# Performance work log

Measured on AMD Instinct MI355X. Metric: run time of the kernel, lower is better.

The kernel has to match this reference:

```python
import jax, jax.numpy as jnp
import numpy as np

B = 262144          # batch
D = 128             # in_dim == out_dim
BS = 16             # block size
K = 8               # number of blocks
RANK = 4            # low-rank blocks' rank
DENSE = np.array([0, 3, 6])   # block ids with mode 'dense'
DIAG = np.array([1, 4, 7])    # block ids with mode 'diagonal'
LR = np.array([2, 5])         # block ids with mode 'lowrank'
EPS = 1e-8


def setup_inputs() -> dict:
    key = jax.random.key(0)
    k1, k2, k3, k4, k5 = jax.random.split(key, 5)
    x = jax.random.normal(k1, (B, D), dtype=jnp.float32)
    # dense blocks: torch init is identity (d_in==d_out); add noise so math is non-trivial
    W_dense = jnp.eye(BS, dtype=jnp.float32)[None] + 0.1 * jax.random.normal(k2, (len(DENSE), BS, BS), dtype=jnp.float32)
    # diagonal blocks: torch init is ones; perturb slightly
    s_diag = 1.0 + 0.1 * jax.random.normal(k3, (len(DIAG), BS), dtype=jnp.float32)
    # lowrank blocks: xavier-uniform-like scale
    lim = float(np.sqrt(6.0 / (BS + RANK)))
    U = jax.random.uniform(k4, (len(LR), BS, RANK), dtype=jnp.float32, minval=-lim, maxval=lim)
    V = jax.random.uniform(k5, (len(LR), BS, RANK), dtype=jnp.float32, minval=-lim, maxval=lim)
    return {"x": x, "W_dense": W_dense, "s_diag": s_diag, "U": U, "V": V}


def reference(x, W_dense, s_diag, U, V):
    # blocks are contiguous [16*j, 16*(j+1)), so gather == reshape to [B, K, BS]
    x3 = x.reshape(B, K, BS)
    # dense blocks: torch Linear y = x @ W.T, W is [d_out, d_in]
    yd = jnp.einsum('bkd,kod->bko', x3[:, DENSE], W_dense)
    # diagonal blocks: elementwise scale
    yg = x3[:, DIAG] * s_diag
    # lowrank blocks: x @ V @ U.T
    yl = jnp.einsum('bkr,kor->bko', jnp.einsum('bkd,kdr->bkr', x3[:, LR], V), U)
    y = jnp.zeros_like(x3).at[:, DENSE].set(yd).at[:, DIAG].set(yg).at[:, LR].set(yl)
    y = y.reshape(B, D)
    # l2 normalize (normalize=True)
    norm = jnp.linalg.norm(y, axis=-1, keepdims=True)
    return y / (norm + EPS)
```

## Files before the change

### kernel.cpp

```cpp
#include <hip/hip_runtime.h>

#define BATCH   262144
#define DDIM    128
#define GRID    2048
#define NITER   8
#define FLUSH   4

template <int CTRL>
__device__ __forceinline__ float fdpp(float v) {
    int i = __builtin_bit_cast(int, v);
    i = __builtin_amdgcn_mov_dpp(i, CTRL, 0xF, 0xF, true);
    return __builtin_bit_cast(float, i);
}
__device__ __forceinline__ float fswz16(float v) {
    int i = __builtin_bit_cast(int, v);
    i = __builtin_amdgcn_ds_swizzle(i, 0x401F);
    return __builtin_bit_cast(float, i);
}

__global__ __launch_bounds__(256, 4) void bdla_kernel(
    const float* __restrict__ x,
    const float* __restrict__ Wd,
    const float* __restrict__ sd,
    const float* __restrict__ U,
    const float* __restrict__ V,
    float* __restrict__ out)
{
    __shared__ float wl[1072];
    __shared__ float obuf[4][FLUSH][4][DDIM];

    const int tid = threadIdx.x;
    for (int i = tid; i < 768; i += 256) wl[i] = Wd[i];
    if (tid < 48)  wl[768 + tid] = sd[tid];
    if (tid < 128) wl[816 + tid] = U[tid];
    if (tid < 128) wl[944 + tid] = V[tid];
    __syncthreads();

    const int lane   = tid & 63;
    const int lane32 = lane & 31;
    const int half   = lane >> 5;
    const int w      = tid >> 6;
    const int j      = lane32 >> 2;
    const int sub    = lane32 & 3;
    const int mode   = j % 3;
    const int k      = j / 3;

    float A[4][16];
    if (mode == 0) {
        const float* wm = &wl[k * 256];
#pragma unroll
        for (int oo = 0; oo < 4; ++oo) {
            const int o = sub * 4 + oo;
#pragma unroll
            for (int m = 0; m < 4; ++m)
#pragma unroll
                for (int c = 0; c < 4; ++c)
                    A[oo][m * 4 + c] = wm[o * 16 + ((sub ^ m) * 4 + c)];
        }
    } else if (mode == 1) {
        const float* s = &wl[768 + k * 16];
#pragma unroll
        for (int oo = 0; oo < 4; ++oo)
#pragma unroll
            for (int m = 0; m < 4; ++m)
#pragma unroll
                for (int c = 0; c < 4; ++c)
                    A[oo][m * 4 + c] = (m == 0 && c == oo) ? s[sub * 4 + oo] : 0.0f;
    } else {
        const float* u = &wl[816 + k * 64];
        const float* v = &wl[944 + k * 64];
#pragma unroll
        for (int oo = 0; oo < 4; ++oo) {
            const int o = sub * 4 + oo;
#pragma unroll
            for (int m = 0; m < 4; ++m)
#pragma unroll
                for (int c = 0; c < 4; ++c) {
                    const int d = (sub ^ m) * 4 + c;
                    float acc = 0.0f;
#pragma unroll
                    for (int r = 0; r < 4; ++r)
                        acc += u[o * 4 + r] * v[d * 4 + r];
                    A[oo][m * 4 + c] = acc;
                }
        }
    }

#pragma unroll
    for (int oo = 0; oo < 4; ++oo)
#pragma unroll
        for (int t = 0; t < 16; ++t)
            asm volatile("" : "+v"(A[oo][t]));

    const int gw = blockIdx.x * 4 + w;
    const float* xbase = x + (size_t)(gw * 4 + half) * DDIM + lane32 * 4;
    const size_t istep = (size_t)(GRID * 4 * 4) * DDIM;

    float4 a0 = *(const float4*)(xbase);
    float4 b0 = *(const float4*)(xbase + 2 * DDIM);
    float4 a1 = *(const float4*)(xbase + istep);
    float4 b1 = *(const float4*)(xbase + istep + 2 * DDIM);

#pragma unroll
    for (int it = 0; it < NITER; ++it) {
        float4 a2, b2;
        if (it + 2 < NITER) {
            a2 = *(const float4*)(xbase + (size_t)(it + 2) * istep);
            b2 = *(const float4*)(xbase + (size_t)(it + 2) * istep + 2 * DDIM);
        }

        float ga[16], gb[16];
        ga[0] = a0.x; ga[1] = a0.y; ga[2] = a0.z; ga[3] = a0.w;
        gb[0] = b0.x; gb[1] = b0.y; gb[2] = b0.z; gb[3] = b0.w;
        ga[4]  = fdpp<0xB1>(a0.x); ga[5]  = fdpp<0xB1>(a0.y);
        ga[6]  = fdpp<0xB1>(a0.z); ga[7]  = fdpp<0xB1>(a0.w);
        gb[4]  = fdpp<0xB1>(b0.x); gb[5]  = fdpp<0xB1>(b0.y);
        gb[6]  = fdpp<0xB1>(b0.z); gb[7]  = fdpp<0xB1>(b0.w);
        ga[8]  = fdpp<0x4E>(a0.x); ga[9]  = fdpp<0x4E>(a0.y);
        ga[10] = fdpp<0x4E>(a0.z); ga[11] = fdpp<0x4E>(a0.w);
        gb[8]  = fdpp<0x4E>(b0.x); gb[9]  = fdpp<0x4E>(b0.y);
        gb[10] = fdpp<0x4E>(b0.z); gb[11] = fdpp<0x4E>(b0.w);
        ga[12] = fdpp<0x1B>(a0.x); ga[13] = fdpp<0x1B>(a0.y);
        ga[14] = fdpp<0x1B>(a0.z); ga[15] = fdpp<0x1B>(a0.w);
        gb[12] = fdpp<0x1B>(b0.x); gb[13] = fdpp<0x1B>(b0.y);
        gb[14] = fdpp<0x1B>(b0.z); gb[15] = fdpp<0x1B>(b0.w);

        float ya0 = 0.f, ya1 = 0.f, ya2 = 0.f, ya3 = 0.f;
        float yb0 = 0.f, yb1 = 0.f, yb2 = 0.f, yb3 = 0.f;
#pragma unroll
        for (int t = 0; t < 16; ++t) {
            ya0 = fmaf(A[0][t], ga[t], ya0);
            ya1 = fmaf(A[1][t], ga[t], ya1);
            ya2 = fmaf(A[2][t], ga[t], ya2);
            ya3 = fmaf(A[3][t], ga[t], ya3);
            yb0 = fmaf(A[0][t], gb[t], yb0);
            yb1 = fmaf(A[1][t], gb[t], yb1);
            yb2 = fmaf(A[2][t], gb[t], yb2);
            yb3 = fmaf(A[3][t], gb[t], yb3);
        }

        float ssa = ya0 * ya0 + ya1 * ya1 + ya2 * ya2 + ya3 * ya3;
        float ssb = yb0 * yb0 + yb1 * yb1 + yb2 * yb2 + yb3 * yb3;
        ssa += fdpp<0xB1>(ssa);  ssb += fdpp<0xB1>(ssb);
        ssa += fdpp<0x4E>(ssa);  ssb += fdpp<0x4E>(ssb);
        ssa += fdpp<0x141>(ssa); ssb += fdpp<0x141>(ssb);
        ssa += fdpp<0x140>(ssa); ssb += fdpp<0x140>(ssb);
        ssa += fswz16(ssa);      ssb += fswz16(ssb);
        const float inva = 1.0f / (sqrtf(ssa) + 1e-8f);
        const float invb = 1.0f / (sqrtf(ssb) + 1e-8f);

        float4 yva, yvb;
        yva.x = ya0 * inva; yva.y = ya1 * inva; yva.z = ya2 * inva; yva.w = ya3 * inva;
        yvb.x = yb0 * invb; yvb.y = yb1 * invb; yvb.z = yb2 * invb; yvb.w = yb3 * invb;

        float* wb = &obuf[w][it & (FLUSH - 1)][0][0];
        *(float4*)(wb + half * DDIM + lane32 * 4)       = yva;
        *(float4*)(wb + (half + 2) * DDIM + lane32 * 4) = yvb;

        if ((it & (FLUSH - 1)) == (FLUSH - 1)) {
            const int f = it >> 2;
#pragma unroll
            for (int s = 0; s < FLUSH; ++s) {
#pragma unroll
                for (int p = 0; p < 2; ++p) {
                    const float4 v =
                        *(const float4*)(&obuf[w][s][p * 2][0] + lane * 4);
                    const size_t row = (size_t)(f * FLUSH + s) * (GRID * 16)
                                     + gw * 4 + p * 2;
                    *(float4*)(out + row * DDIM + lane * 4) = v;
                }
            }
        }

        a0 = a1; b0 = b1; a1 = a2; b1 = b2;
    }
}

extern "C" void kernel_launch(void* const* d_in, const int* in_sizes, int n_in,
                              void* d_out, int out_size, void* d_ws, size_t ws_size,
                              hipStream_t stream) {
    const float* x  = (const float*)d_in[0];
    const float* Wd = (const float*)d_in[1];
    const float* sd = (const float*)d_in[2];
    const float* U  = (const float*)d_in[3];
    const float* V  = (const float*)d_in[4];
    float* out = (float*)d_out;
    (void)in_sizes; (void)n_in; (void)out_size; (void)d_ws; (void)ws_size;

    dim3 grid(GRID), block(256);
    hipLaunchKernelGGL(bdla_kernel, grid, block, 0, stream, x, Wd, sd, U, V, out);
}
```

Baseline: 280.7 us.

## Batch input loads into two phases of four and prefetch before weight setup

```diff
diff --git a/kernel.cpp b/kernel.cpp
--- a/kernel.cpp
+++ b/kernel.cpp
@@ -4,7 +4,7 @@
 #define DDIM    128
 #define GRID    2048
 #define NITER   8
-#define FLUSH   4
+#define PH      4
 
 template <int CTRL>
 __device__ __forceinline__ float fdpp(float v) {
@@ -18,7 +18,57 @@
     return __builtin_bit_cast(float, i);
 }
 
-__global__ __launch_bounds__(256, 4) void bdla_kernel(
+#define BDLA_BODY(A0, B0, WB)                                                 \
+    {                                                                         \
+        const float4 a0 = (A0);                                               \
+        const float4 b0 = (B0);                                               \
+        float ga[16], gb[16];                                                 \
+        ga[0] = a0.x; ga[1] = a0.y; ga[2] = a0.z; ga[3] = a0.w;               \
+        gb[0] = b0.x; gb[1] = b0.y; gb[2] = b0.z; gb[3] = b0.w;               \
+        ga[4]  = fdpp<0xB1>(a0.x); ga[5]  = fdpp<0xB1>(a0.y);                 \
+        ga[6]  = fdpp<0xB1>(a0.z); ga[7]  = fdpp<0xB1>(a0.w);                 \
+        gb[4]  = fdpp<0xB1>(b0.x); gb[5]  = fdpp<0xB1>(b0.y);                 \
+        gb[6]  = fdpp<0xB1>(b0.z); gb[7]  = fdpp<0xB1>(b0.w);                 \
+        ga[8]  = fdpp<0x4E>(a0.x); ga[9]  = fdpp<0x4E>(a0.y);                 \
+        ga[10] = fdpp<0x4E>(a0.z); ga[11] = fdpp<0x4E>(a0.w);                 \
+        gb[8]  = fdpp<0x4E>(b0.x); gb[9]  = fdpp<0x4E>(b0.y);                 \
+        gb[10] = fdpp<0x4E>(b0.z); gb[11] = fdpp<0x4E>(b0.w);                 \
+        ga[12] = fdpp<0x1B>(a0.x); ga[13] = fdpp<0x1B>(a0.y);                 \
+        ga[14] = fdpp<0x1B>(a0.z); ga[15] = fdpp<0x1B>(a0.w);                 \
+        gb[12] = fdpp<0x1B>(b0.x); gb[13] = fdpp<0x1B>(b0.y);                 \
+        gb[14] = fdpp<0x1B>(b0.z); gb[15] = fdpp<0x1B>(b0.w);                 \
+        float ya0 = 0.f, ya1 = 0.f, ya2 = 0.f, ya3 = 0.f;                     \
+        float yb0 = 0.f, yb1 = 0.f, yb2 = 0.f, yb3 = 0.f;                     \
+        _Pragma("unroll")                                                     \
+        for (int t = 0; t < 16; ++t) {                                        \
+            ya0 = fmaf(A[0][t], ga[t], ya0);                                  \
+            ya1 = fmaf(A[1][t], ga[t], ya1);                                  \
+            ya2 = fmaf(A[2][t], ga[t], ya2);                                  \
+            ya3 = fmaf(A[3][t], ga[t], ya3);                                  \
+            yb0 = fmaf(A[0][t], gb[t], yb0);                                  \
+            yb1 = fmaf(A[1][t], gb[t], yb1);                                  \
+            yb2 = fmaf(A[2][t], gb[t], yb2);                                  \
+            yb3 = fmaf(A[3][t], gb[t], yb3);                                  \
+        }                                                                     \
+        float ssa = ya0 * ya0 + ya1 * ya1 + ya2 * ya2 + ya3 * ya3;            \
+        float ssb = yb0 * yb0 + yb1 * yb1 + yb2 * yb2 + yb3 * yb3;            \
+        ssa += fdpp<0xB1>(ssa);  ssb += fdpp<0xB1>(ssb);                      \
+        ssa += fdpp<0x4E>(ssa);  ssb += fdpp<0x4E>(ssb);                      \
+        ssa += fdpp<0x141>(ssa); ssb += fdpp<0x141>(ssb);                     \
+        ssa += fdpp<0x140>(ssa); ssb += fdpp<0x140>(ssb);                     \
+        ssa += fswz16(ssa);      ssb += fswz16(ssb);                          \
+        const float inva = 1.0f / (sqrtf(ssa) + 1e-8f);                       \
+        const float invb = 1.0f / (sqrtf(ssb) + 1e-8f);                       \
+        float4 yva, yvb;                                                      \
+        yva.x = ya0 * inva; yva.y = ya1 * inva;                               \
+        yva.z = ya2 * inva; yva.w = ya3 * inva;                               \
+        yvb.x = yb0 * invb; yvb.y = yb1 * invb;                               \
+        yvb.z = yb2 * invb; yvb.w = yb3 * invb;                               \
+        *(float4*)((WB) + half * DDIM + lane32 * 4)       = yva;              \
+        *(float4*)((WB) + (half + 2) * DDIM + lane32 * 4) = yvb;              \
+    }
+
+__global__ __launch_bounds__(256, 3) void bdla_kernel(
     const float* __restrict__ x,
     const float* __restrict__ Wd,
     const float* __restrict__ sd,
@@ -27,7 +77,7 @@
     float* __restrict__ out)
 {
     __shared__ float wl[1072];
-    __shared__ float obuf[4][FLUSH][4][DDIM];
+    __shared__ float obuf[4][PH][4][DDIM];
 
     const int tid = threadIdx.x;
     for (int i = tid; i < 768; i += 256) wl[i] = Wd[i];
@@ -45,6 +95,17 @@
     const int mode   = j % 3;
     const int k      = j / 3;
 
+    const int gw = blockIdx.x * 4 + w;
+    const float* xbase = x + (size_t)(gw * 4 + half) * DDIM + lane32 * 4;
+    const size_t istep = (size_t)(GRID * 4 * 4) * DDIM;
+
+    float4 pa[PH], pb[PH];
+#pragma unroll
+    for (int s = 0; s < PH; ++s) {
+        pa[s] = *(const float4*)(xbase + (size_t)s * istep);
+        pb[s] = *(const float4*)(xbase + (size_t)s * istep + 2 * DDIM);
+    }
+
     float A[4][16];
     if (mode == 0) {
         const float* wm = &wl[k * 256];
@@ -85,94 +146,42 @@
                 }
         }
     }
-
 #pragma unroll
     for (int oo = 0; oo < 4; ++oo)
 #pragma unroll
         for (int t = 0; t < 16; ++t)
             asm volatile("" : "+v"(A[oo][t]));
 
-    const int gw = blockIdx.x * 4 + w;
-    const float* xbase = x + (size_t)(gw * 4 + half) * DDIM + lane32 * 4;
-    const size_t istep = (size_t)(GRID * 4 * 4) * DDIM;
-
-    float4 a0 = *(const float4*)(xbase);
-    float4 b0 = *(const float4*)(xbase + 2 * DDIM);
-    float4 a1 = *(const float4*)(xbase + istep);
-    float4 b1 = *(const float4*)(xbase + istep + 2 * DDIM);
-
-#pragma unroll
-    for (int it = 0; it < NITER; ++it) {
-        float4 a2, b2;
-        if (it + 2 < NITER) {
-            a2 = *(const float4*)(xbase + (size_t)(it + 2) * istep);
-            b2 = *(const float4*)(xbase + (size_t)(it + 2) * istep + 2 * DDIM);
-        }
-
-        float ga[16], gb[16];
-        ga[0] = a0.x; ga[1] = a0.y; ga[2] = a0.z; ga[3] = a0.w;
-        gb[0] = b0.x; gb[1] = b0.y; gb[2] = b0.z; gb[3] = b0.w;
-        ga[4]  = fdpp<0xB1>(a0.x); ga[5]  = fdpp<0xB1>(a0.y);
-        ga[6]  = fdpp<0xB1>(a0.z); ga[7]  = fdpp<0xB1>(a0.w);
-        gb[4]  = fdpp<0xB1>(b0.x); gb[5]  = fdpp<0xB1>(b0.y);
-        gb[6]  = fdpp<0xB1>(b0.z); gb[7]  = fdpp<0xB1>(b0.w);
-        ga[8]  = fdpp<0x4E>(a0.x); ga[9]  = fdpp<0x4E>(a0.y);
-        ga[10] = fdpp<0x4E>(a0.z); ga[11] = fdpp<0x4E>(a0.w);
-        gb[8]  = fdpp<0x4E>(b0.x); gb[9]  = fdpp<0x4E>(b0.y);
-        gb[10] = fdpp<0x4E>(b0.z); gb[11] = fdpp<0x4E>(b0.w);
-        ga[12] = fdpp<0x1B>(a0.x); ga[13] = fdpp<0x1B>(a0.y);
-        ga[14] = fdpp<0x1B>(a0.z); ga[15] = fdpp<0x1B>(a0.w);
-        gb[12] = fdpp<0x1B>(b0.x); gb[13] = fdpp<0x1B>(b0.y);
-        gb[14] = fdpp<0x1B>(b0.z); gb[15] = fdpp<0x1B>(b0.w);
-
-        float ya0 = 0.f, ya1 = 0.f, ya2 = 0.f, ya3 = 0.f;
-        float yb0 = 0.f, yb1 = 0.f, yb2 = 0.f, yb3 = 0.f;
-#pragma unroll
-        for (int t = 0; t < 16; ++t) {
-            ya0 = fmaf(A[0][t], ga[t], ya0);
-            ya1 = fmaf(A[1][t], ga[t], ya1);
-            ya2 = fmaf(A[2][t], ga[t], ya2);
-            ya3 = fmaf(A[3][t], ga[t], ya3);
-            yb0 = fmaf(A[0][t], gb[t], yb0);
-            yb1 = fmaf(A[1][t], gb[t], yb1);
-            yb2 = fmaf(A[2][t], gb[t], yb2);
-            yb3 = fmaf(A[3][t], gb[t], yb3);
-        }
-
-        float ssa = ya0 * ya0 + ya1 * ya1 + ya2 * ya2 + ya3 * ya3;
-        float ssb = yb0 * yb0 + yb1 * yb1 + yb2 * yb2 + yb3 * yb3;
-        ssa += fdpp<0xB1>(ssa);  ssb += fdpp<0xB1>(ssb);
-        ssa += fdpp<0x4E>(ssa);  ssb += fdpp<0x4E>(ssb);
-        ssa += fdpp<0x141>(ssa); ssb += fdpp<0x141>(ssb);
-        ssa += fdpp<0x140>(ssa); ssb += fdpp<0x140>(ssb);
-        ssa += fswz16(ssa);      ssb += fswz16(ssb);
-        const float inva = 1.0f / (sqrtf(ssa) + 1e-8f);
-        const float invb = 1.0f / (sqrtf(ssb) + 1e-8f);
-
-        float4 yva, yvb;
-        yva.x = ya0 * inva; yva.y = ya1 * inva; yva.z = ya2 * inva; yva.w = ya3 * inva;
-        yvb.x = yb0 * invb; yvb.y = yb1 * invb; yvb.z = yb2 * invb; yvb.w = yb3 * invb;
-
-        float* wb = &obuf[w][it & (FLUSH - 1)][0][0];
-        *(float4*)(wb + half * DDIM + lane32 * 4)       = yva;
-        *(float4*)(wb + (half + 2) * DDIM + lane32 * 4) = yvb;
-
-        if ((it & (FLUSH - 1)) == (FLUSH - 1)) {
-            const int f = it >> 2;
-#pragma unroll
-            for (int s = 0; s < FLUSH; ++s) {
-#pragma unroll
-                for (int p = 0; p < 2; ++p) {
-                    const float4 v =
-                        *(const float4*)(&obuf[w][s][p * 2][0] + lane * 4);
-                    const size_t row = (size_t)(f * FLUSH + s) * (GRID * 16)
-                                     + gw * 4 + p * 2;
-                    *(float4*)(out + row * DDIM + lane * 4) = v;
-                }
-            }
-        }
-
-        a0 = a1; b0 = b1; a1 = a2; b1 = b2;
+#pragma unroll
+    for (int it = 0; it < PH; ++it)
+        BDLA_BODY(pa[it], pb[it], &obuf[w][it][0][0]);
+
+#pragma unroll
+    for (int s = 0; s < PH; ++s) {
+        pa[s] = *(const float4*)(xbase + (size_t)(PH + s) * istep);
+        pb[s] = *(const float4*)(xbase + (size_t)(PH + s) * istep + 2 * DDIM);
+    }
+
+#pragma unroll
+    for (int s = 0; s < PH; ++s) {
+        const size_t rowbase = (size_t)s * (GRID * 16) + gw * 4;
+        const float4 v0 = *(const float4*)(&obuf[w][s][0][0] + lane * 4);
+        const float4 v1 = *(const float4*)(&obuf[w][s][2][0] + lane * 4);
+        *(float4*)(out + rowbase * DDIM + lane * 4)       = v0;
+        *(float4*)(out + (rowbase + 2) * DDIM + lane * 4) = v1;
+    }
+
+#pragma unroll
+    for (int it = 0; it < PH; ++it)
+        BDLA_BODY(pa[it], pb[it], &obuf[w][it][0][0]);
+
+#pragma unroll
+    for (int s = 0; s < PH; ++s) {
+        const size_t rowbase = (size_t)(PH + s) * (GRID * 16) + gw * 4;
+        const float4 v0 = *(const float4*)(&obuf[w][s][0][0] + lane * 4);
+        const float4 v1 = *(const float4*)(&obuf[w][s][2][0] + lane * 4);
+        *(float4*)(out + rowbase * DDIM + lane * 4)       = v0;
+        *(float4*)(out + (rowbase + 2) * DDIM + lane * 4) = v1;
     }
 }
 
```

Result: no change. 279.5 us (-0.4%).
